# Performance work log

Measured on AMD Instinct MI355X. Metric: run time of the kernel, lower is better.

## Reference

```python
import jax, jax.numpy as jnp
import numpy as np

U = 8          # units per modular layer
B = 16384      # batch
IN = 512       # input feature dim
H = 512        # modular hidden dim
NC = 62        # n_class


def _aggregate(P, h):
    # P: [T, F] policy link matrix; h: [F, B, D] per-unit features.
    # agg[t] = sum_f P[t,f] * h[f], normalized by row-sum when row-sum > 0.
    s = jnp.einsum('tf,fbd->tbd', P, h)
    row = P.sum(axis=1)                      # [T]
    safe = jnp.where(row > 0, row, 1.0)[:, None, None]
    return jnp.where((row > 0)[:, None, None], s / safe, s)


def setup_inputs() -> dict:
    key = jax.random.key(0)
    ks = jax.random.split(key, 12)
    s_in = 1.0 / np.sqrt(IN)
    s_h = 1.0 / np.sqrt(H)
    return {
        'x': jax.random.normal(ks[0], (B, IN), jnp.float32),
        'policy1': jax.random.uniform(ks[1], (U * U,), jnp.float32),
        'policy2': jax.random.uniform(ks[2], (U * U,), jnp.float32),
        'policy_final': jax.random.uniform(ks[3], (U,), jnp.float32),
        'W0': jax.random.uniform(ks[4], (U, IN, H), jnp.float32, -s_in, s_in),
        'b0': jax.random.uniform(ks[5], (U, H), jnp.float32, -s_in, s_in),
        'W1': jax.random.uniform(ks[6], (U, H, H), jnp.float32, -s_h, s_h),
        'b1': jax.random.uniform(ks[7], (U, H), jnp.float32, -s_h, s_h),
        'W2': jax.random.uniform(ks[8], (U, H, NC), jnp.float32, -s_h, s_h),
        'b2': jax.random.uniform(ks[9], (U, NC), jnp.float32, -s_h, s_h),
    }


def reference(x, policy1, policy2, policy_final, W0, b0, W1, b1, W2, b2):
    # Layer 0 (input modular layer): policy_list[0] is forced to all-ones,
    # so every unit sees x unscaled. Each unit: Linear + ReLU.
    h0 = jax.nn.relu(jnp.einsum('bi,uid->ubd', x, W0) + b0[:, None, :])  # [U,B,H]

    # Mid layer: policy-gated weighted-sum aggregation, then per-unit Linear+ReLU.
    a1 = _aggregate(policy1.reshape(U, U), h0)
    h1 = jax.nn.relu(jnp.einsum('ubi,uid->ubd', a1, W1) + b1[:, None, :])

    # Output modular layer: aggregate then per-unit Linear (no activation).
    a2 = _aggregate(policy2.reshape(U, U), h1)
    h2 = jnp.einsum('ubi,uic->ubc', a2, W2) + b2[:, None, :]  # [U,B,NC]

    # Final gating. Original code divides by divider INSIDE the unit loop
    # (every iteration), so replicate that recurrence exactly.
    d = policy_final.sum()
    inv = jnp.where(d > 0, 1.0 / jnp.where(d > 0, d, 1.0), 1.0)
    out = jnp.zeros((B, NC), jnp.float32)
    for j in range(U):  # fixed small unit count, not a data dim
        out = (out + h2[j] * policy_final[j]) * inv
    return out
```

## Files before the change

kernel.cpp:

```cpp
#include <hip/hip_runtime.h>

#define U_   8
#define B_   16384
#define NC_  62

typedef __attribute__((ext_vector_type(8))) short bfrag;
typedef __attribute__((ext_vector_type(4))) float facc;

__device__ __forceinline__ float bf2f(unsigned int lo16) {
    union { unsigned int i; float f; } v;
    v.i = lo16 << 16;
    return v.f;
}
__device__ __forceinline__ unsigned short f2bf(float f) {
    unsigned int x = __float_as_uint(f);
    return (unsigned short)((x + 0x7fffu + ((x >> 16) & 1u)) >> 16);
}
__device__ __forceinline__ void gl2lds16(const void* g, void* l) {
    __builtin_amdgcn_global_load_lds(
        (const __attribute__((address_space(1))) void*)g,
        (__attribute__((address_space(3))) void*)l, 16, 0, 0);
}
__device__ __forceinline__ void cfence() { asm volatile("" ::: "memory"); }
__device__ __forceinline__ void bar() {
    asm volatile("" ::: "memory");
    __builtin_amdgcn_s_barrier();
    asm volatile("" ::: "memory");
}
__device__ __forceinline__ void barL() {
    asm volatile("s_waitcnt lgkmcnt(0)" ::: "memory");
    __builtin_amdgcn_s_barrier();
    asm volatile("" ::: "memory");
}
#define VMCNT(n) asm volatile("s_waitcnt vmcnt(" #n ")" ::: "memory")

__global__ void prep_kernel(const float* __restrict__ p1, const float* __restrict__ p2,
                            const float* __restrict__ pf, const float* __restrict__ b2,
                            float* __restrict__ P1n, float* __restrict__ P2n,
                            float* __restrict__ wfin, float* __restrict__ cconst)
{
    int t = threadIdx.x;
    if (t >= 64) return;
    int row = t >> 3;
    float s1 = 0.f, s2 = 0.f;
    for (int f = 0; f < 8; f++) { s1 += p1[row * 8 + f]; s2 += p2[row * 8 + f]; }
    P1n[t] = p1[t] * (s1 > 0.f ? 1.f / s1 : 1.f);
    P2n[t] = p2[t] * (s2 > 0.f ? 1.f / s2 : 1.f);
    float d = 0.f;
    for (int j = 0; j < 8; j++) d += pf[j];
    float inv = d > 0.f ? 1.f / d : 1.f;
    float wv[8];
    for (int j = 0; j < 8; j++) {
        float v = pf[j];
        for (int i = j; i < 8; i++) v *= inv;
        wv[j] = v;
    }
    if (t < 8) wfin[t] = wv[t];
    float cc = 0.f;
    if (t < NC_) for (int u = 0; u < 8; u++) cc += wv[u] * b2[u * NC_ + t];
    cconst[t] = cc;
}

__global__ __launch_bounds__(256) void reorder_w0(
    const float* __restrict__ W0, unsigned short* __restrict__ W0r)
{
    __shared__ float tile[32][33];
    const int u  = blockIdx.z;
    const int n0 = blockIdx.x * 32, k0 = blockIdx.y * 32;
    const int tx = threadIdx.x & 31, ty = threadIdx.x >> 5;
    const float* Wb = W0 + (long)u * 512 * 512;
#pragma unroll
    for (int i = 0; i < 4; i++)
        tile[ty + i * 8][tx] = Wb[(long)(k0 + ty + i * 8) * 512 + n0 + tx];
    __syncthreads();
#pragma unroll
    for (int i = 0; i < 4; i++) {
        int n = n0 + ty + i * 8, k = k0 + tx;
        int np = (n >> 5) * 256 + u * 32 + (n & 31);
        W0r[(long)np * 512 + k] = f2bf(tile[tx][ty + i * 8]);
    }
}

__global__ __launch_bounds__(256) void transpose_w(
    const float* __restrict__ W, unsigned short* __restrict__ Wt)
{
    __shared__ float tile[32][33];
    const int u  = blockIdx.z;
    const int n0 = blockIdx.x * 32, k0 = blockIdx.y * 32;
    const int tx = threadIdx.x & 31, ty = threadIdx.x >> 5;
    const float* Wb = W + (long)u * 512 * 512;
#pragma unroll
    for (int i = 0; i < 4; i++)
        tile[ty + i * 8][tx] = Wb[(long)(k0 + ty + i * 8) * 512 + n0 + tx];
    __syncthreads();
    unsigned short* Wo = Wt + (long)u * 512 * 512;
#pragma unroll
    for (int i = 0; i < 4; i++) {
        int n = n0 + ty + i * 8, k = k0 + tx;
        Wo[(long)n * 512 + k] = f2bf(tile[tx][ty + i * 8]);
    }
}

__global__ __launch_bounds__(256) void wout_build(
    const float* __restrict__ W2, const float* __restrict__ P2n,
    const float* __restrict__ wfin, unsigned short* __restrict__ Woutt)
{
    const int c   = threadIdx.x & 63;
    const int row = blockIdx.x * 4 + (threadIdx.x >> 6);
    const int f = row >> 9, k = row & 511;
    float s = 0.f;
    if (c < NC_) {
#pragma unroll
        for (int u = 0; u < 8; u++)
            s += wfin[u] * P2n[u * 8 + f] * W2[((long)u * 512 + k) * NC_ + c];
    }
    Woutt[(long)c * 4096 + row] = f2bf(s);
}

__global__ __launch_bounds__(256) void convert_x(
    const float* __restrict__ x, unsigned short* __restrict__ xb, long n)
{
    long i = ((long)blockIdx.x * 256 + threadIdx.x) * 8;
    if (i >= n) return;
    const float4* xp = (const float4*)(x + i);
    float4 a = xp[0], b = xp[1];
    uint4 o;
    o.x = f2bf(a.x) | ((unsigned)f2bf(a.y) << 16);
    o.y = f2bf(a.z) | ((unsigned)f2bf(a.w) << 16);
    o.z = f2bf(b.x) | ((unsigned)f2bf(b.y) << 16);
    o.w = f2bf(b.z) | ((unsigned)f2bf(b.w) << 16);
    *(uint4*)(xb + i) = o;
}

__global__ __launch_bounds__(256, 2) void gemm0_mix(
    const unsigned short* __restrict__ xb, const unsigned short* __restrict__ W0r,
    const float* __restrict__ b0, const float* __restrict__ P1n,
    unsigned short* __restrict__ a1, long plane)
{
    __shared__ __align__(16) unsigned short sm[33792];
    const int tid = threadIdx.x, w = tid >> 6, lane = tid & 63;
    const int flat = blockIdx.x;
    const int xcd = flat & 7, seq = flat >> 3;
    const int ng = xcd * 2 + (seq & 1);
    const long mBase = (long)(seq >> 1) * 128;

    const int lr = lane >> 2;
    const int lg = (lane & 3) ^ ((lane >> 3) & 3);
    const int wm = w >> 1, wn = w & 1;
    const int r = lane & 15, q = lane >> 4;
    const int xq = (q ^ ((r >> 1) & 3)) * 8;

    facc acc[4][8];
#pragma unroll
    for (int i = 0; i < 4; i++)
#pragma unroll
        for (int j = 0; j < 8; j++) acc[i][j] = (facc){0.f, 0.f, 0.f, 0.f};

    auto stage = [&](int buf, int kt) {
        const int k0 = kt * 32;
        unsigned short* dA = sm + buf * 4096;
        unsigned short* dB = sm + 8192 + buf * 8192;
#pragma unroll
        for (int i = 0; i < 2; i++) {
            const int c = w * 2 + i;
            gl2lds16(xb + (mBase + c * 16 + lr) * 512 + k0 + lg * 8, dA + c * 512);
        }
#pragma unroll
        for (int i = 0; i < 4; i++) {
            const int c = w * 4 + i;
            gl2lds16(W0r + ((long)ng * 256 + c * 16 + lr) * 512 + k0 + lg * 8,
                     dB + c * 512);
        }
    };
    auto compute = [&](int buf) {
        const unsigned short* sA = sm + buf * 4096;
        const unsigned short* sB = sm + 8192 + buf * 8192;
        bfrag aF[4], bF[8];
#pragma unroll
        for (int mt = 0; mt < 4; mt++)
            aF[mt] = *(const bfrag*)&sA[(wm * 64 + mt * 16 + r) * 32 + xq];
#pragma unroll
        for (int nt = 0; nt < 8; nt++)
            bF[nt] = *(const bfrag*)&sB[(wn * 128 + nt * 16 + r) * 32 + xq];
#pragma unroll
        for (int mt = 0; mt < 4; mt++)
#pragma unroll
            for (int nt = 0; nt < 8; nt++)
                acc[mt][nt] = __builtin_amdgcn_mfma_f32_16x16x32_bf16(
                    aF[mt], bF[nt], acc[mt][nt], 0, 0, 0);
    };

    stage(0, 0);
    cfence();
    stage(1, 1);
    VMCNT(6);
    bar();
#pragma unroll
    for (int t = 0; t < 16; ++t) {
        compute(t & 1);
        if (t <= 13) {
            barL();
            stage(t & 1, t + 2);
            VMCNT(6);
            bar();
        } else if (t == 14) {
            VMCNT(0);
            bar();
        } else {
            barL();
        }
    }

#pragma unroll
    for (int nt = 0; nt < 8; nt++) {
        const int cl = wn * 128 + nt * 16 + r;
        const float bv = b0[(cl >> 5) * 512 + ng * 32 + (cl & 31)];
#pragma unroll
        for (int mt = 0; mt < 4; mt++) {
            const int rowb = wm * 64 + mt * 16 + q * 4;
#pragma unroll
            for (int rg = 0; rg < 4; rg++) {
                float v = acc[mt][nt][rg] + bv;
                v = v > 0.f ? v : 0.f;
                sm[(rowb + rg) * 264 + cl] = f2bf(v);
            }
        }
    }
    __syncthreads();

    float pw[64];
#pragma unroll
    for (int i = 0; i < 64; i++) pw[i] = P1n[i];
    const int row = tid >> 1, fs0 = (tid & 1) * 16;
    float hv[8][16];
#pragma unroll
    for (int u = 0; u < 8; u++) {
        bfrag ha = *(const bfrag*)&sm[row * 264 + u * 32 + fs0];
        bfrag hb = *(const bfrag*)&sm[row * 264 + u * 32 + fs0 + 8];
#pragma unroll
        for (int j = 0; j < 8; j++) {
            hv[u][j]     = bf2f((unsigned int)(unsigned short)ha[j]);
            hv[u][j + 8] = bf2f((unsigned int)(unsigned short)hb[j]);
        }
    }
    const long rowOff = (mBase + row) * 512 + ng * 32 + fs0;
#pragma unroll
    for (int t = 0; t < 8; t++) {
        float o[16];
#pragma unroll
        for (int j = 0; j < 16; j++) {
            float s = 0.f;
#pragma unroll
            for (int u = 0; u < 8; u++) s = fmaf(pw[t * 8 + u], hv[u][j], s);
            o[j] = s;
        }
        uint4 ov0, ov1;
        ov0.x = f2bf(o[0])  | ((unsigned)f2bf(o[1])  << 16);
        ov0.y = f2bf(o[2])  | ((unsigned)f2bf(o[3])  << 16);
        ov0.z = f2bf(o[4])  | ((unsigned)f2bf(o[5])  << 16);
        ov0.w = f2bf(o[6])  | ((unsigned)f2bf(o[7])  << 16);
        ov1.x = f2bf(o[8])  | ((unsigned)f2bf(o[9])  << 16);
        ov1.y = f2bf(o[10]) | ((unsigned)f2bf(o[11]) << 16);
        ov1.z = f2bf(o[12]) | ((unsigned)f2bf(o[13]) << 16);
        ov1.w = f2bf(o[14]) | ((unsigned)f2bf(o[15]) << 16);
        *(uint4*)(a1 + (long)t * plane + rowOff)     = ov0;
        *(uint4*)(a1 + (long)t * plane + rowOff + 8) = ov1;
    }
}

__global__ __launch_bounds__(256, 2) void gemm_h(
    const unsigned short* __restrict__ a1,
    const unsigned short* __restrict__ W1t,
    const float* __restrict__ b1,
    unsigned short* __restrict__ h1, long plane)
{
    __shared__ __align__(16) unsigned short sm[36864];
    const int tid = threadIdx.x, w = tid >> 6, lane = tid & 63;
    const int flat = blockIdx.x;
    const int u = flat & 7, seq = flat >> 3;
    const long mBase = (long)seq * 64;

    const int lr = lane >> 2;
    const int lg = (lane & 3) ^ ((lane >> 3) & 3);
    const int r = lane & 15, q = lane >> 4;
    const int xq = (q ^ ((r >> 1) & 3)) * 8;

    const unsigned short* Ab = a1 + (long)u * plane;
    const unsigned short* Bb = W1t + (long)u * 512 * 512;

    facc acc[4][8];
#pragma unroll
    for (int i = 0; i < 4; i++)
#pragma unroll
        for (int j = 0; j < 8; j++) acc[i][j] = (facc){0.f, 0.f, 0.f, 0.f};

    auto stage = [&](int buf, int kt) {
        const int k0 = kt * 32;
        unsigned short* dA = sm + buf * 2048;
        unsigned short* dB = sm + 4096 + buf * 16384;
        gl2lds16(Ab + (mBase + w * 16 + lr) * 512 + k0 + lg * 8, dA + w * 512);
#pragma unroll
        for (int i = 0; i < 8; i++) {
            const int c = w * 8 + i;
            gl2lds16(Bb + (long)(c * 16 + lr) * 512 + k0 + lg * 8, dB + c * 512);
        }
    };
    auto compute = [&](int buf) {
        const unsigned short* sA = sm + buf * 2048;
        const unsigned short* sB = sm + 4096 + buf * 16384;
        bfrag aF[4], bF[8];
#pragma unroll
        for (int mt = 0; mt < 4; mt++)
            aF[mt] = *(const bfrag*)&sA[(mt * 16 + r) * 32 + xq];
#pragma unroll
        for (int nt = 0; nt < 8; nt++)
            bF[nt] = *(const bfrag*)&sB[(w * 128 + nt * 16 + r) * 32 + xq];
#pragma unroll
        for (int mt = 0; mt < 4; mt++)
#pragma unroll
            for (int nt = 0; nt < 8; nt++)
                acc[mt][nt] = __builtin_amdgcn_mfma_f32_16x16x32_bf16(
                    aF[mt], bF[nt], acc[mt][nt], 0, 0, 0);
    };

    stage(0, 0);
    cfence();
    stage(1, 1);
    VMCNT(9);
    bar();
#pragma unroll
    for (int t = 0; t < 16; ++t) {
        compute(t & 1);
        if (t <= 13) {
            barL();
            stage(t & 1, t + 2);
            VMCNT(9);
            bar();
        } else if (t == 14) {
            VMCNT(0);
            bar();
        } else {
            barL();
        }
    }

#pragma unroll
    for (int nt = 0; nt < 8; nt++) {
        const int col = w * 128 + nt * 16 + r;
        const float bv = b1[u * 512 + col];
#pragma unroll
        for (int mt = 0; mt < 4; mt++) {
            const int rowb = mt * 16 + q * 4;
#pragma unroll
            for (int rg = 0; rg < 4; rg++) {
                float v = acc[mt][nt][rg] + bv;
                v = v > 0.f ? v : 0.f;
                sm[(rowb + rg) * 520 + col] = f2bf(v);
            }
        }
    }
    __syncthreads();

    unsigned short* Cb = h1 + (long)u * plane + mBase * 512;
#pragma unroll
    for (int it = 0; it < 16; it++) {
        const int g = tid + it * 256;
        const int row = g >> 6, gr = g & 63;
        *(uint4*)(Cb + (long)row * 512 + gr * 8) = *(const uint4*)&sm[row * 520 + gr * 8];
    }
}

__global__ __launch_bounds__(256, 1) void gemm_out(
    const unsigned short* __restrict__ h1,
    const unsigned short* __restrict__ Bt,
    float* __restrict__ partial, long plane, int Bc)
{
    __shared__ __align__(16) unsigned short sm[16384];
    const int tid = threadIdx.x, w = tid >> 6, lane = tid & 63;
    const int flat = blockIdx.x;
    const int kc = flat & 1;
    const long mBase = (long)(flat >> 1) * 64;

    const int lr = lane >> 3, lg = (lane & 7) ^ lr;
    const int wm = w >> 1, wn = w & 1;
    const int r = lane & 15, q = lane >> 4;
    const int x7 = r & 7;

    facc acc[2][2];
#pragma unroll
    for (int i = 0; i < 2; i++)
#pragma unroll
        for (int j = 0; j < 2; j++) acc[i][j] = (facc){0.f, 0.f, 0.f, 0.f};

    auto stage = [&](int buf, int it) {
        const int u = kc * 4 + (it >> 3);
        const int kk = (it & 7) * 64;
        unsigned short* dA = sm + buf * 4096;
        unsigned short* dB = sm + 8192 + buf * 4096;
#pragma unroll
        for (int i = 0; i < 2; i++) {
            const int c = w * 2 + i;
            gl2lds16(h1 + (long)u * plane + (mBase + c * 8 + lr) * 512 + kk + lg * 8,
                     dA + c * 512);
            gl2lds16(Bt + (long)(c * 8 + lr) * 4096 + u * 512 + kk + lg * 8,
                     dB + c * 512);
        }
    };
    auto compute = [&](int buf) {
        const unsigned short* sA = sm + buf * 4096;
        const unsigned short* sB = sm + 8192 + buf * 4096;
#pragma unroll
        for (int h = 0; h < 2; h++) {
            const int xg = ((h * 4 + q) ^ x7) * 8;
            bfrag aF[2], bF[2];
#pragma unroll
            for (int mt = 0; mt < 2; mt++)
                aF[mt] = *(const bfrag*)&sA[(wm * 32 + mt * 16 + r) * 64 + xg];
#pragma unroll
            for (int nt = 0; nt < 2; nt++)
                bF[nt] = *(const bfrag*)&sB[(wn * 32 + nt * 16 + r) * 64 + xg];
#pragma unroll
            for (int mt = 0; mt < 2; mt++)
#pragma unroll
                for (int nt = 0; nt < 2; nt++)
                    acc[mt][nt] = __builtin_amdgcn_mfma_f32_16x16x32_bf16(
                        aF[mt], bF[nt], acc[mt][nt], 0, 0, 0);
        }
    };

    stage(0, 0);
    cfence();
    stage(1, 1);
    VMCNT(4);
    bar();
#pragma unroll
    for (int t = 0; t < 32; ++t) {
        compute(t & 1);
        if (t <= 29) {
            barL();
            stage(t & 1, t + 2);
            VMCNT(4);
            bar();
        } else if (t == 30) {
            VMCNT(0);
            bar();
        }
    }

    float* pb = partial + ((long)kc * Bc + mBase) * 64;
#pragma unroll
    for (int nt = 0; nt < 2; nt++) {
        const int col = wn * 32 + nt * 16 + r;
#pragma unroll
        for (int mt = 0; mt < 2; mt++) {
#pragma unroll
            for (int rg = 0; rg < 4; rg++) {
                const int row = wm * 32 + mt * 16 + q * 4 + rg;
                pb[(long)row * 64 + col] = acc[mt][nt][rg];
            }
        }
    }
}

__global__ __launch_bounds__(256) void reduce_out(
    const float* __restrict__ partial, const float* __restrict__ cconst,
    float* __restrict__ out, int Bc)
{
    const long flat = (long)blockIdx.x * 256 + threadIdx.x;
    const long row = flat >> 2;
    const int cg = (int)(flat & 3) * 16;
    float s[16];
#pragma unroll
    for (int j = 0; j < 16; j++) s[j] = 0.f;
#pragma unroll
    for (int kc = 0; kc < 2; kc++) {
        const float4* p = (const float4*)(partial + ((long)kc * Bc + row) * 64 + cg);
#pragma unroll
        for (int v4 = 0; v4 < 4; v4++) {
            float4 v = p[v4];
            s[v4 * 4 + 0] += v.x; s[v4 * 4 + 1] += v.y;
            s[v4 * 4 + 2] += v.z; s[v4 * 4 + 3] += v.w;
        }
    }
#pragma unroll
    for (int j = 0; j < 16; j++) {
        const int c = cg + j;
        if (c < NC_) out[row * NC_ + c] = s[j] + cconst[c];
    }
}

extern "C" void kernel_launch(void* const* d_in, const int* in_sizes, int n_in,
                              void* d_out, int out_size, void* d_ws, size_t ws_size,
                              hipStream_t stream)
{
    const float* x  = (const float*)d_in[0];
    const float* p1 = (const float*)d_in[1];
    const float* p2 = (const float*)d_in[2];
    const float* pf = (const float*)d_in[3];
    const float* W0 = (const float*)d_in[4];
    const float* b0 = (const float*)d_in[5];
    const float* W1 = (const float*)d_in[6];
    const float* b1 = (const float*)d_in[7];
    const float* W2 = (const float*)d_in[8];
    const float* b2 = (const float*)d_in[9];
    float* out = (float*)d_out;

    char* ws = (char*)d_ws;
    size_t off = 0;
    auto alloc = [&](size_t bytes) -> void* {
        void* p = ws + off;
        off += (bytes + 255) & ~(size_t)255;
        return p;
    };
    float* P1n    = (float*)alloc(64 * sizeof(float));
    float* P2n    = (float*)alloc(64 * sizeof(float));
    float* wfin   = (float*)alloc(8 * sizeof(float));
    float* cconst = (float*)alloc(64 * sizeof(float));
    unsigned short* W0r   = (unsigned short*)alloc((size_t)4096 * 512 * 2);
    unsigned short* W1t   = (unsigned short*)alloc((size_t)U_ * 512 * 512 * 2);
    unsigned short* Woutt = (unsigned short*)alloc((size_t)64 * 4096 * 2);
    unsigned short* xb    = (unsigned short*)alloc((size_t)B_ * 512 * 2);

    size_t remain = ws_size > off ? ws_size - off : 0;
    int Bc = 2048;
    for (int cand = B_; cand >= 2048; cand >>= 1) {
        size_t need = 2ull * 8 * cand * 512 * 2 + 2ull * cand * 64 * 4 + 1024;
        if (need <= remain) { Bc = cand; break; }
    }
    unsigned short* a1 = (unsigned short*)alloc(8ull * Bc * 512 * 2);
    unsigned short* h1 = (unsigned short*)alloc(8ull * Bc * 512 * 2);
    float* partial     = (float*)alloc(2ull * Bc * 64 * 4);

    prep_kernel<<<1, 64, 0, stream>>>(p1, p2, pf, b2, P1n, P2n, wfin, cconst);
    reorder_w0<<<dim3(16, 16, 8), 256, 0, stream>>>(W0, W0r);
    transpose_w<<<dim3(16, 16, 8), 256, 0, stream>>>(W1, W1t);
    wout_build<<<dim3(1024), 256, 0, stream>>>(W2, P2n, wfin, Woutt);
    convert_x<<<dim3(B_ * 512 / 8 / 256), 256, 0, stream>>>(x, xb, (long)B_ * 512);

    const int Mb = Bc / 128;
    const long plane = (long)Bc * 512;
    for (int bb = 0; bb < B_; bb += Bc) {
        gemm0_mix<<<dim3(16 * Mb), 256, 0, stream>>>(
            xb + (long)bb * 512, W0r, b0, P1n, a1, plane);
        gemm_h<<<dim3(8 * (Bc / 64)), 256, 0, stream>>>(a1, W1t, b1, h1, plane);
        gemm_out<<<dim3(2 * (Bc / 64)), 256, 0, stream>>>(h1, Woutt, partial, plane, Bc);
        reduce_out<<<dim3(Bc / 64), 256, 0, stream>>>(
            partial, cconst, out + (long)bb * NC_, Bc);
    }
}
```

Before: 350.4 us.

## Fuse output GEMM into hidden GEMM epilogue and merge prep kernels

Combines the five preprocessing kernels (policy normalisation, weight reorders, output-weight build, x conversion) into a single launch, with the policy normalisation recomputed inline in the consumers. The second modular GEMM now keeps its ReLU tile in LDS and multiplies it directly by the per-unit slice of the combined output weight, writing per-unit partial sums. This removes the h1 round-trip through global memory and the separate gemm_out launch. In exchange there are 8 partial planes instead of 2 for reduce_out to sum, a larger LDS footprint, and some redundant scalar work per thread.

```diff
diff --git a/kernel.cpp b/kernel.cpp
--- a/kernel.cpp
+++ b/kernel.cpp
@@ -33,108 +33,86 @@
     asm volatile("" ::: "memory");
 }
 #define VMCNT(n) asm volatile("s_waitcnt vmcnt(" #n ")" ::: "memory")
-
-__global__ void prep_kernel(const float* __restrict__ p1, const float* __restrict__ p2,
-                            const float* __restrict__ pf, const float* __restrict__ b2,
-                            float* __restrict__ P1n, float* __restrict__ P2n,
-                            float* __restrict__ wfin, float* __restrict__ cconst)
-{
-    int t = threadIdx.x;
-    if (t >= 64) return;
-    int row = t >> 3;
-    float s1 = 0.f, s2 = 0.f;
-    for (int f = 0; f < 8; f++) { s1 += p1[row * 8 + f]; s2 += p2[row * 8 + f]; }
-    P1n[t] = p1[t] * (s1 > 0.f ? 1.f / s1 : 1.f);
-    P2n[t] = p2[t] * (s2 > 0.f ? 1.f / s2 : 1.f);
-    float d = 0.f;
-    for (int j = 0; j < 8; j++) d += pf[j];
-    float inv = d > 0.f ? 1.f / d : 1.f;
-    float wv[8];
-    for (int j = 0; j < 8; j++) {
-        float v = pf[j];
-        for (int i = j; i < 8; i++) v *= inv;
-        wv[j] = v;
-    }
-    if (t < 8) wfin[t] = wv[t];
-    float cc = 0.f;
-    if (t < NC_) for (int u = 0; u < 8; u++) cc += wv[u] * b2[u * NC_ + t];
-    cconst[t] = cc;
-}
-
-__global__ __launch_bounds__(256) void reorder_w0(
-    const float* __restrict__ W0, unsigned short* __restrict__ W0r)
+#define LGKM0()  asm volatile("s_waitcnt lgkmcnt(0)" ::: "memory")
+
+__global__ __launch_bounds__(256) void prep_all(
+    const float* __restrict__ p2, const float* __restrict__ pf,
+    const float* __restrict__ W0, const float* __restrict__ W1,
+    const float* __restrict__ W2, const float* __restrict__ x,
+    unsigned short* __restrict__ W0r, unsigned short* __restrict__ W1t,
+    unsigned short* __restrict__ Woutt, unsigned short* __restrict__ xb)
 {
     __shared__ float tile[32][33];
-    const int u  = blockIdx.z;
-    const int n0 = blockIdx.x * 32, k0 = blockIdx.y * 32;
-    const int tx = threadIdx.x & 31, ty = threadIdx.x >> 5;
-    const float* Wb = W0 + (long)u * 512 * 512;
-#pragma unroll
-    for (int i = 0; i < 4; i++)
-        tile[ty + i * 8][tx] = Wb[(long)(k0 + ty + i * 8) * 512 + n0 + tx];
-    __syncthreads();
-#pragma unroll
-    for (int i = 0; i < 4; i++) {
-        int n = n0 + ty + i * 8, k = k0 + tx;
-        int np = (n >> 5) * 256 + u * 32 + (n & 31);
-        W0r[(long)np * 512 + k] = f2bf(tile[tx][ty + i * 8]);
-    }
-}
-
-__global__ __launch_bounds__(256) void transpose_w(
-    const float* __restrict__ W, unsigned short* __restrict__ Wt)
-{
-    __shared__ float tile[32][33];
-    const int u  = blockIdx.z;
-    const int n0 = blockIdx.x * 32, k0 = blockIdx.y * 32;
-    const int tx = threadIdx.x & 31, ty = threadIdx.x >> 5;
-    const float* Wb = W + (long)u * 512 * 512;
-#pragma unroll
-    for (int i = 0; i < 4; i++)
-        tile[ty + i * 8][tx] = Wb[(long)(k0 + ty + i * 8) * 512 + n0 + tx];
-    __syncthreads();
-    unsigned short* Wo = Wt + (long)u * 512 * 512;
-#pragma unroll
-    for (int i = 0; i < 4; i++) {
-        int n = n0 + ty + i * 8, k = k0 + tx;
-        Wo[(long)n * 512 + k] = f2bf(tile[tx][ty + i * 8]);
-    }
-}
-
-__global__ __launch_bounds__(256) void wout_build(
-    const float* __restrict__ W2, const float* __restrict__ P2n,
-    const float* __restrict__ wfin, unsigned short* __restrict__ Woutt)
-{
-    const int c   = threadIdx.x & 63;
-    const int row = blockIdx.x * 4 + (threadIdx.x >> 6);
-    const int f = row >> 9, k = row & 511;
-    float s = 0.f;
-    if (c < NC_) {
-#pragma unroll
-        for (int u = 0; u < 8; u++)
-            s += wfin[u] * P2n[u * 8 + f] * W2[((long)u * 512 + k) * NC_ + c];
-    }
-    Woutt[(long)c * 4096 + row] = f2bf(s);
-}
-
-__global__ __launch_bounds__(256) void convert_x(
-    const float* __restrict__ x, unsigned short* __restrict__ xb, long n)
-{
-    long i = ((long)blockIdx.x * 256 + threadIdx.x) * 8;
-    if (i >= n) return;
-    const float4* xp = (const float4*)(x + i);
-    float4 a = xp[0], b = xp[1];
-    uint4 o;
-    o.x = f2bf(a.x) | ((unsigned)f2bf(a.y) << 16);
-    o.y = f2bf(a.z) | ((unsigned)f2bf(a.w) << 16);
-    o.z = f2bf(b.x) | ((unsigned)f2bf(b.y) << 16);
-    o.w = f2bf(b.z) | ((unsigned)f2bf(b.w) << 16);
-    *(uint4*)(xb + i) = o;
+    const int b = blockIdx.x;
+
+    if (b < 4096) {
+        const bool isW0 = (b < 2048);
+        const int bb = isW0 ? b : b - 2048;
+        const int u  = bb >> 8;
+        const int n0 = (bb & 15) * 32, k0 = ((bb >> 4) & 15) * 32;
+        const int tx = threadIdx.x & 31, ty = threadIdx.x >> 5;
+        const float* Wb = (isW0 ? W0 : W1) + (long)u * 512 * 512;
+#pragma unroll
+        for (int i = 0; i < 4; i++)
+            tile[ty + i * 8][tx] = Wb[(long)(k0 + ty + i * 8) * 512 + n0 + tx];
+        __syncthreads();
+        if (isW0) {
+#pragma unroll
+            for (int i = 0; i < 4; i++) {
+                int n = n0 + ty + i * 8, k = k0 + tx;
+                int np = (n >> 5) * 256 + u * 32 + (n & 31);
+                W0r[(long)np * 512 + k] = f2bf(tile[tx][ty + i * 8]);
+            }
+        } else {
+            unsigned short* Wo = W1t + (long)u * 512 * 512;
+#pragma unroll
+            for (int i = 0; i < 4; i++) {
+                int n = n0 + ty + i * 8, k = k0 + tx;
+                Wo[(long)n * 512 + k] = f2bf(tile[tx][ty + i * 8]);
+            }
+        }
+    } else if (b < 5120) {
+        const int bx = b - 4096;
+        const int c   = threadIdx.x & 63;
+        const int row = bx * 4 + (threadIdx.x >> 6);
+        const int f = row >> 9, k = row & 511;
+        float d = 0.f;
+#pragma unroll
+        for (int j = 0; j < 8; j++) d += pf[j];
+        float inv = d > 0.f ? 1.f / d : 1.f;
+        float s = 0.f;
+        if (c < NC_) {
+#pragma unroll
+            for (int u = 0; u < 8; u++) {
+                float wv = pf[u];
+#pragma unroll
+                for (int i = u; i < 8; i++) wv *= inv;
+                float s2 = 0.f;
+#pragma unroll
+                for (int ff = 0; ff < 8; ff++) s2 += p2[u * 8 + ff];
+                float p2n = p2[u * 8 + f] * (s2 > 0.f ? 1.f / s2 : 1.f);
+                s += wv * p2n * W2[((long)u * 512 + k) * NC_ + c];
+            }
+        }
+        Woutt[(long)c * 4096 + row] = f2bf(s);
+    } else {
+        const int bx = b - 5120;
+        long i = ((long)bx * 256 + threadIdx.x) * 8;
+        if (i >= (long)B_ * 512) return;
+        const float4* xp = (const float4*)(x + i);
+        float4 a = xp[0], bb4 = xp[1];
+        uint4 o;
+        o.x = f2bf(a.x) | ((unsigned)f2bf(a.y) << 16);
+        o.y = f2bf(a.z) | ((unsigned)f2bf(a.w) << 16);
+        o.z = f2bf(bb4.x) | ((unsigned)f2bf(bb4.y) << 16);
+        o.w = f2bf(bb4.z) | ((unsigned)f2bf(bb4.w) << 16);
+        *(uint4*)(xb + i) = o;
+    }
 }
 
 __global__ __launch_bounds__(256, 2) void gemm0_mix(
     const unsigned short* __restrict__ xb, const unsigned short* __restrict__ W0r,
-    const float* __restrict__ b0, const float* __restrict__ P1n,
+    const float* __restrict__ b0, const float* __restrict__ p1,
     unsigned short* __restrict__ a1, long plane)
 {
     __shared__ __align__(16) unsigned short sm[33792];
@@ -230,7 +208,14 @@
 
     float pw[64];
 #pragma unroll
-    for (int i = 0; i < 64; i++) pw[i] = P1n[i];
+    for (int t8 = 0; t8 < 8; t8++) {
+        float s1 = 0.f;
+#pragma unroll
+        for (int f = 0; f < 8; f++) s1 += p1[t8 * 8 + f];
+        float inv = s1 > 0.f ? 1.f / s1 : 1.f;
+#pragma unroll
+        for (int f = 0; f < 8; f++) pw[t8 * 8 + f] = p1[t8 * 8 + f] * inv;
+    }
     const int row = tid >> 1, fs0 = (tid & 1) * 16;
     float hv[8][16];
 #pragma unroll
@@ -268,17 +253,19 @@
     }
 }
 
-__global__ __launch_bounds__(256, 2) void gemm_h(
+__global__ __launch_bounds__(256, 2) void gemm_hout(
     const unsigned short* __restrict__ a1,
     const unsigned short* __restrict__ W1t,
     const float* __restrict__ b1,
-    unsigned short* __restrict__ h1, long plane)
+    const unsigned short* __restrict__ Woutt,
+    float* __restrict__ partial, long plane)
 {
-    __shared__ __align__(16) unsigned short sm[36864];
+    __shared__ __align__(16) unsigned short sm[37504];
     const int tid = threadIdx.x, w = tid >> 6, lane = tid & 63;
     const int flat = blockIdx.x;
     const int u = flat & 7, seq = flat >> 3;
     const long mBase = (long)seq * 64;
+    const long Bc = plane >> 9;
 
     const int lr = lane >> 2;
     const int lg = (lane & 3) ^ ((lane >> 3) & 3);
@@ -355,116 +342,61 @@
             for (int rg = 0; rg < 4; rg++) {
                 float v = acc[mt][nt][rg] + bv;
                 v = v > 0.f ? v : 0.f;
-                sm[(rowb + rg) * 520 + col] = f2bf(v);
+                sm[(rowb + rg) * 522 + col] = f2bf(v);
             }
         }
     }
     __syncthreads();
 
-    unsigned short* Cb = h1 + (long)u * plane + mBase * 512;
-#pragma unroll
-    for (int it = 0; it < 16; it++) {
-        const int g = tid + it * 256;
-        const int row = g >> 6, gr = g & 63;
-        *(uint4*)(Cb + (long)row * 512 + gr * 8) = *(const uint4*)&sm[row * 520 + gr * 8];
-    }
-}
-
-__global__ __launch_bounds__(256, 1) void gemm_out(
-    const unsigned short* __restrict__ h1,
-    const unsigned short* __restrict__ Bt,
-    float* __restrict__ partial, long plane, int Bc)
-{
-    __shared__ __align__(16) unsigned short sm[16384];
-    const int tid = threadIdx.x, w = tid >> 6, lane = tid & 63;
-    const int flat = blockIdx.x;
-    const int kc = flat & 1;
-    const long mBase = (long)(flat >> 1) * 64;
-
-    const int lr = lane >> 3, lg = (lane & 7) ^ lr;
-    const int wm = w >> 1, wn = w & 1;
-    const int r = lane & 15, q = lane >> 4;
-    const int x7 = r & 7;
-
-    facc acc[2][2];
-#pragma unroll
-    for (int i = 0; i < 2; i++)
-#pragma unroll
-        for (int j = 0; j < 2; j++) acc[i][j] = (facc){0.f, 0.f, 0.f, 0.f};
-
-    auto stage = [&](int buf, int it) {
-        const int u = kc * 4 + (it >> 3);
-        const int kk = (it & 7) * 64;
-        unsigned short* dA = sm + buf * 4096;
-        unsigned short* dB = sm + 8192 + buf * 4096;
-#pragma unroll
-        for (int i = 0; i < 2; i++) {
-            const int c = w * 2 + i;
-            gl2lds16(h1 + (long)u * plane + (mBase + c * 8 + lr) * 512 + kk + lg * 8,
-                     dA + c * 512);
-            gl2lds16(Bt + (long)(c * 8 + lr) * 4096 + u * 512 + kk + lg * 8,
-                     dB + c * 512);
-        }
-    };
-    auto compute = [&](int buf) {
-        const unsigned short* sA = sm + buf * 4096;
-        const unsigned short* sB = sm + 8192 + buf * 4096;
-#pragma unroll
-        for (int h = 0; h < 2; h++) {
-            const int xg = ((h * 4 + q) ^ x7) * 8;
-            bfrag aF[2], bF[2];
-#pragma unroll
-            for (int mt = 0; mt < 2; mt++)
-                aF[mt] = *(const bfrag*)&sA[(wm * 32 + mt * 16 + r) * 64 + xg];
-#pragma unroll
-            for (int nt = 0; nt < 2; nt++)
-                bF[nt] = *(const bfrag*)&sB[(wn * 32 + nt * 16 + r) * 64 + xg];
-#pragma unroll
-            for (int mt = 0; mt < 2; mt++)
-#pragma unroll
-                for (int nt = 0; nt < 2; nt++)
-                    acc[mt][nt] = __builtin_amdgcn_mfma_f32_16x16x32_bf16(
-                        aF[mt], bF[nt], acc[mt][nt], 0, 0, 0);
-        }
-    };
-
-    stage(0, 0);
+    unsigned short* Wb0 = sm + 33408;
+    const unsigned short* Wg = Woutt + (long)u * 512;
+
+    facc acc2[4];
+#pragma unroll
+    for (int i = 0; i < 4; i++) acc2[i] = (facc){0.f, 0.f, 0.f, 0.f};
+
+    auto stage2 = [&](int buf, int kt) {
+        gl2lds16(Wg + (long)(w * 16 + lr) * 4096 + kt * 32 + lg * 8,
+                 Wb0 + buf * 2048 + w * 512);
+    };
+    auto compute2 = [&](int buf, int kt) {
+        const unsigned short* sW = Wb0 + buf * 2048;
+        bfrag bW = *(const bfrag*)&sW[(w * 16 + r) * 32 + xq];
+#pragma unroll
+        for (int mt = 0; mt < 4; mt++) {
+            bfrag aH = *(const bfrag*)&sm[(mt * 16 + r) * 522 + kt * 32 + q * 8];
+            acc2[mt] = __builtin_amdgcn_mfma_f32_16x16x32_bf16(
+                aH, bW, acc2[mt], 0, 0, 0);
+        }
+    };
+
+    stage2(0, 0);
     cfence();
-    stage(1, 1);
-    VMCNT(4);
-    bar();
-#pragma unroll
-    for (int t = 0; t < 32; ++t) {
-        compute(t & 1);
-        if (t <= 29) {
-            barL();
-            stage(t & 1, t + 2);
-            VMCNT(4);
-            bar();
-        } else if (t == 30) {
-            VMCNT(0);
-            bar();
-        }
-    }
-
-    float* pb = partial + ((long)kc * Bc + mBase) * 64;
-#pragma unroll
-    for (int nt = 0; nt < 2; nt++) {
-        const int col = wn * 32 + nt * 16 + r;
-#pragma unroll
-        for (int mt = 0; mt < 2; mt++) {
-#pragma unroll
-            for (int rg = 0; rg < 4; rg++) {
-                const int row = wm * 32 + mt * 16 + q * 4 + rg;
-                pb[(long)row * 64 + col] = acc[mt][nt][rg];
-            }
+    stage2(1, 1);
+#pragma unroll
+    for (int t = 0; t < 16; ++t) {
+        if (t < 15) { VMCNT(1); } else { VMCNT(0); }
+        compute2(t & 1, t);
+        if (t <= 13) {
+            LGKM0();
+            stage2(t & 1, t + 2);
+        }
+    }
+
+    float* pb = partial + ((long)u * Bc + mBase) * 64;
+#pragma unroll
+    for (int mt = 0; mt < 4; mt++) {
+#pragma unroll
+        for (int rg = 0; rg < 4; rg++) {
+            const int prow = mt * 16 + q * 4 + rg;
+            pb[(long)prow * 64 + w * 16 + r] = acc2[mt][rg];
         }
     }
 }
 
 __global__ __launch_bounds__(256) void reduce_out(
-    const float* __restrict__ partial, const float* __restrict__ cconst,
-    float* __restrict__ out, int Bc)
+    const float* __restrict__ partial, const float* __restrict__ pf,
+    const float* __restrict__ b2, float* __restrict__ out, int Bc)
 {
     const long flat = (long)blockIdx.x * 256 + threadIdx.x;
     const long row = flat >> 2;
@@ -473,8 +405,8 @@
 #pragma unroll
     for (int j = 0; j < 16; j++) s[j] = 0.f;
 #pragma unroll
-    for (int kc = 0; kc < 2; kc++) {
-        const float4* p = (const float4*)(partial + ((long)kc * Bc + row) * 64 + cg);
+    for (int u = 0; u < 8; u++) {
+        const float4* p = (const float4*)(partial + ((long)u * Bc + row) * 64 + cg);
 #pragma unroll
         for (int v4 = 0; v4 < 4; v4++) {
             float4 v = p[v4];
@@ -482,10 +414,27 @@
             s[v4 * 4 + 2] += v.z; s[v4 * 4 + 3] += v.w;
         }
     }
+    float d = 0.f;
+#pragma unroll
+    for (int j = 0; j < 8; j++) d += pf[j];
+    float inv = d > 0.f ? 1.f / d : 1.f;
+    float wv[8];
+#pragma unroll
+    for (int j = 0; j < 8; j++) {
+        float v = pf[j];
+#pragma unroll
+        for (int i = j; i < 8; i++) v *= inv;
+        wv[j] = v;
+    }
 #pragma unroll
     for (int j = 0; j < 16; j++) {
         const int c = cg + j;
-        if (c < NC_) out[row * NC_ + c] = s[j] + cconst[c];
+        if (c < NC_) {
+            float cc = 0.f;
+#pragma unroll
+            for (int u = 0; u < 8; u++) cc += wv[u] * b2[u * NC_ + c];
+            out[row * NC_ + c] = s[j] + cc;
+        }
     }
 }
 
@@ -512,10 +461,6 @@
         off += (bytes + 255) & ~(size_t)255;
         return p;
     };
-    float* P1n    = (float*)alloc(64 * sizeof(float));
-    float* P2n    = (float*)alloc(64 * sizeof(float));
-    float* wfin   = (float*)alloc(8 * sizeof(float));
-    float* cconst = (float*)alloc(64 * sizeof(float));
     unsigned short* W0r   = (unsigned short*)alloc((size_t)4096 * 512 * 2);
     unsigned short* W1t   = (unsigned short*)alloc((size_t)U_ * 512 * 512 * 2);
     unsigned short* Woutt = (unsigned short*)alloc((size_t)64 * 4096 * 2);
@@ -524,27 +469,23 @@
     size_t remain = ws_size > off ? ws_size - off : 0;
     int Bc = 2048;
     for (int cand = B_; cand >= 2048; cand >>= 1) {
-        size_t need = 2ull * 8 * cand * 512 * 2 + 2ull * cand * 64 * 4 + 1024;
+        size_t need = 8ull * cand * 512 * 2 + 8ull * cand * 64 * 4 + 1024;
         if (need <= remain) { Bc = cand; break; }
     }
     unsigned short* a1 = (unsigned short*)alloc(8ull * Bc * 512 * 2);
-    unsigned short* h1 = (unsigned short*)alloc(8ull * Bc * 512 * 2);
-    float* partial     = (float*)alloc(2ull * Bc * 64 * 4);
-
-    prep_kernel<<<1, 64, 0, stream>>>(p1, p2, pf, b2, P1n, P2n, wfin, cconst);
-    reorder_w0<<<dim3(16, 16, 8), 256, 0, stream>>>(W0, W0r);
-    transpose_w<<<dim3(16, 16, 8), 256, 0, stream>>>(W1, W1t);
-    wout_build<<<dim3(1024), 256, 0, stream>>>(W2, P2n, wfin, Woutt);
-    convert_x<<<dim3(B_ * 512 / 8 / 256), 256, 0, stream>>>(x, xb, (long)B_ * 512);
+    float* partial     = (float*)alloc(8ull * Bc * 64 * 4);
+
+    prep_all<<<dim3(9216), 256, 0, stream>>>(
+        p2, pf, W0, W1, W2, x, W0r, W1t, Woutt, xb);
 
     const int Mb = Bc / 128;
     const long plane = (long)Bc * 512;
     for (int bb = 0; bb < B_; bb += Bc) {
         gemm0_mix<<<dim3(16 * Mb), 256, 0, stream>>>(
-            xb + (long)bb * 512, W0r, b0, P1n, a1, plane);
-        gemm_h<<<dim3(8 * (Bc / 64)), 256, 0, stream>>>(a1, W1t, b1, h1, plane);
-        gemm_out<<<dim3(2 * (Bc / 64)), 256, 0, stream>>>(h1, Woutt, partial, plane, Bc);
+            xb + (long)bb * 512, W0r, b0, p1, a1, plane);
+        gemm_hout<<<dim3(8 * (Bc / 64)), 256, 0, stream>>>(
+            a1, W1t, b1, Woutt, partial, plane);
         reduce_out<<<dim3(Bc / 64), 256, 0, stream>>>(
-            partial, cconst, out + (long)bb * NC_, Bc);
-    }
-}
+            partial, pf, b2, out + (long)bb * NC_, Bc);
+    }
+}
```

Result: faster. 307.5 us (-12.2%).
